# Kernel optimization log

Hardware: AMD Instinct MI355X
Metric: run time of the kernel (lower is better)

## Reference

```python
import jax, jax.numpy as jnp
import numpy as np

N = 4096   # nodes
D = 512    # feature dim
E = 65536  # edges
HOPS = 10  # APPNP K (init arg 'hops')
ALPHA = 0.5


def setup_inputs() -> dict:
    key = jax.random.key(0)
    k1, k2, k3 = jax.random.split(key, 3)
    x_train = jax.random.normal(k1, (N, D), dtype=jnp.float32)
    # kernel_scale = nn.Linear(D, 1, bias=False) weight, flattened to [D]
    w = jax.random.normal(k2, (D,), dtype=jnp.float32) * 0.05
    edge_index = jax.random.randint(k3, (2, E), 0, N, dtype=jnp.int32)
    return {"x_train": x_train, "w": w, "edge_index": edge_index}


def appnp(x0, src, dst, hops, alpha):
    # torch_geometric APPNP with gcn_norm (add self-loops, symmetric norm), dropout=0
    n = x0.shape[0]
    loop = jnp.arange(n, dtype=src.dtype)
    s = jnp.concatenate([src, loop])
    d = jnp.concatenate([dst, loop])
    deg = jax.ops.segment_sum(jnp.ones_like(s, dtype=x0.dtype), d, num_segments=n)
    dis = deg ** -0.5  # deg >= 1 thanks to self-loops
    norm = dis[s] * dis[d]

    def body(h, _):
        agg = jax.ops.segment_sum(norm[:, None] * h[s], d, num_segments=n)
        return (1.0 - alpha) * agg + alpha * x0, None

    h, _ = jax.lax.scan(body, x0, None, length=hops)
    return h


def reference(x_train, w, edge_index):
    n = x_train.shape[0]
    # RBF_kernel: K[i,j] = sum_d w_d * (x_i - x_j)_d^2 for i != j, diag = 1 (the eye)
    xw = x_train * w                                   # [N, D]
    sq = jnp.sum(xw * x_train, axis=1)                 # [N] weighted squared norms
    K = sq[:, None] + sq[None, :] - 2.0 * (xw @ x_train.T)  # [N, N]
    idx = jnp.arange(n)
    K = K.at[idx, idx].set(1.0)

    src, dst = edge_index[0], edge_index[1]
    kgg = appnp(K, src, dst, HOPS, ALPHA)
    kgg = appnp(kgg.T, src, dst, HOPS, ALPHA)

    # adj = dense coo(edge_index, ones); diag = (diag(adj.sum(dim=1)) + 1) ** -0.5
    # (adds 1 to the WHOLE matrix, so off-diagonal entries become 1.0 -- faithful)
    deg_row = jax.ops.segment_sum(jnp.ones((edge_index.shape[1],), K.dtype), src, num_segments=n)
    Dmat = (jnp.diag(deg_row) + 1.0) ** -0.5           # [N, N]
    kgg = Dmat * kgg       # elementwise, as in the original
    kgg = Dmat * kgg.T
    return kgg
```

## Files before the change

### kernel.cpp

```cpp
#include <hip/hip_runtime.h>
#include <stdint.h>

#define Nn 4096
#define Dd 512
#define Ee 65536
#define HOPS 10
#define TPB 512
#define RPT (Nn / TPB)
#define CT8 8
#define WCAP 64
#define KEXT 1536
#define YC 640
#define XK 8192
#define NTMM 88

typedef short bf16x8 __attribute__((ext_vector_type(8)));
typedef float f32x4 __attribute__((ext_vector_type(4)));

__device__ __forceinline__ unsigned short bf16r(float x) {
  unsigned int b = __float_as_uint(x);
  return (unsigned short)((b + 0x7FFFu + ((b >> 16) & 1u)) >> 16);
}
__device__ __forceinline__ unsigned int pkbf(float lo, float hi) {
  return (unsigned int)bf16r(lo) | ((unsigned int)bf16r(hi) << 16);
}
__device__ __forceinline__ float ubf(unsigned short h) {
  return __uint_as_float(((unsigned int)h) << 16);
}
__device__ __forceinline__ void gld16(const unsigned short* g, unsigned short* lds) {
  __builtin_amdgcn_global_load_lds(
      (const __attribute__((address_space(1))) unsigned int*)g,
      (__attribute__((address_space(3))) unsigned int*)lds, 16, 0, 0);
}

__global__ __launch_bounds__(256) void k_sq(const float* __restrict__ x,
                                            const float* __restrict__ w,
                                            float* __restrict__ sq) {
  int row = blockIdx.x;
  int tid = threadIdx.x;
  const float* xr = x + (size_t)row * Dd;
  float partial = 0.f;
  for (int d = tid; d < Dd; d += 256) {
    float xv = xr[d];
    partial += xv * xv * w[d];
  }
  for (int off = 32; off >= 1; off >>= 1) partial += __shfl_down(partial, off, 64);
  __shared__ float red[4];
  int wv = tid >> 6, ln = tid & 63;
  if (ln == 0) red[wv] = partial;
  __syncthreads();
  if (tid == 0) sq[row] = red[0] + red[1] + red[2] + red[3];
}

__global__ void k_count(const int* __restrict__ src, const int* __restrict__ dst,
                        int* __restrict__ degi, int* __restrict__ degrow) {
  int e = blockIdx.x * blockDim.x + threadIdx.x;
  if (e < Ee) {
    atomicAdd(&degi[dst[e]], 1);
    atomicAdd(&degrow[src[e]], 1);
  }
}

__global__ void k_dis(const int* __restrict__ degi, const int* __restrict__ degrow,
                      float* __restrict__ dis, float* __restrict__ d2) {
  int i = blockIdx.x * 256 + threadIdx.x;
  dis[i] = rsqrtf((float)(degi[i] + 1));
  d2[i] = 1.0f / ((float)degrow[i] + 1.0f);
}

__global__ void k_hist(const int* __restrict__ degi, int* __restrict__ binbase) {
  __shared__ int h[WCAP + 1];
  int t = threadIdx.x;
  if (t <= WCAP) h[t] = 0;
  __syncthreads();
  for (int i = t; i < Nn; i += 256) {
    int d = degi[i] + 1;
    if (d > WCAP) d = WCAP;
    atomicAdd(&h[d], 1);
  }
  __syncthreads();
  if (t == 0) {
    int run = 0;
    for (int b = 0; b <= WCAP; b++) { int c = h[b]; binbase[b] = run; run += c; }
  }
}

__global__ void k_scatter(const int* __restrict__ degi, const int* __restrict__ binbase,
                          int* __restrict__ bincnt, int* __restrict__ perm,
                          int* __restrict__ rnk) {
  int i = blockIdx.x * 256 + threadIdx.x;
  int d = degi[i] + 1;
  if (d > WCAP) d = WCAP;
  int pos = binbase[d] + atomicAdd(&bincnt[d], 1);
  perm[pos] = i;
  rnk[i] = pos;
}

__global__ void k_wsub(const int* __restrict__ degi, const int* __restrict__ perm,
                       int* __restrict__ wsub) {
  int t = threadIdx.x;
  int d = degi[perm[t * 64 + 63]] + 1;
  wsub[t] = d > WCAP ? WCAP : d;
}

__global__ void k_fill_ell(const int* __restrict__ src, const int* __restrict__ dst,
                           const float* __restrict__ dis, const int* __restrict__ rnk,
                           int* __restrict__ slot, int2* __restrict__ ell) {
  int i = blockIdx.x * blockDim.x + threadIdx.x;
  if (i < Ee) {
    int s = src[i], d = dst[i];
    int p = atomicAdd(&slot[d], 1);
    if (p < WCAP) ell[(size_t)p * Nn + rnk[d]] = make_int2(s, __float_as_int(dis[s] * dis[d]));
  } else if (i < Ee + Nn) {
    int v = i - Ee;
    int p = atomicAdd(&slot[v], 1);
    if (p < WCAP) ell[(size_t)p * Nn + rnk[v]] = make_int2(v, __float_as_int(dis[v] * dis[v]));
  }
}

__global__ __launch_bounds__(256) void k_xpose(const float* __restrict__ x,
                                               unsigned short* __restrict__ xb) {
  __shared__ float tile[32][33];
  int cx = blockIdx.x, rx = blockIdx.y;
  int t = threadIdx.x, txc = t & 31, tyc = t >> 5;
#pragma unroll
  for (int i = 0; i < 4; i++) {
    int a = tyc + i * 8;
    tile[a][txc] = x[(size_t)(rx * 32 + a) * Dd + cx * 32 + txc];
  }
  __syncthreads();
#pragma unroll
  for (int i = 0; i < 4; i++) {
    int a = tyc + i * 8;
    int c = cx * 32 + a;
    float v = tile[txc][a];
    unsigned short hi = bf16r(v);
    xb[(size_t)c * XK + rx * 32 + txc] = hi;
    xb[(size_t)c * XK + Nn + rx * 32 + txc] = bf16r(v - ubf(hi));
  }
}

__global__ void k_tail(const float* __restrict__ sq, unsigned short* __restrict__ xb) {
  int r = blockIdx.x * 256 + threadIdx.x;
  float v = sq[r];
  unsigned short hi = bf16r(v);
  xb[(size_t)512 * XK + r] = hi;
  xb[(size_t)512 * XK + Nn + r] = bf16r(v - ubf(hi));
  xb[(size_t)513 * XK + r] = bf16r(1.0f);
  xb[(size_t)513 * XK + Nn + r] = 0;
}

__global__ __launch_bounds__(TPB, 4) void k_appnp(unsigned short* __restrict__ mb,
                                                  const int2* __restrict__ ell,
                                                  const int* __restrict__ perm,
                                                  const int* __restrict__ wsub) {
  extern __shared__ uint4 h4u[];
  int j0 = blockIdx.x * CT8;
  int tid = threadIdx.x;
  int wv = tid >> 6, ln = tid & 63;
  int qb = wv * 512 + ln;

#pragma unroll
  for (int rr = 0; rr < RPT; rr++) {
    int r = tid + rr * TPB;
    uint4 v = make_uint4(0u, 0u, 0u, 0u);
    int c = r - j0;
    if (c >= 0 && c < 8) {
      unsigned int one = (c & 1) ? 0x3F800000u : 0x00003F80u;
      if ((c >> 1) == 0) v.x = one;
      else if ((c >> 1) == 1) v.y = one;
      else if ((c >> 1) == 2) v.z = one;
      else v.w = one;
    }
    h4u[r] = v;
  }

  int ws[RPT];
#pragma unroll
  for (int rr = 0; rr < RPT; rr++)
    ws[rr] = __builtin_amdgcn_readfirstlane(wsub[wv * 8 + rr]);
  const int Wv = ws[RPT - 1];

  int rp[RPT], x0c[RPT];
#pragma unroll
  for (int rr = 0; rr < RPT; rr++) {
    rp[rr] = perm[qb + rr * 64];
    int c = rp[rr] - j0;
    x0c[rr] = (c >= 0 && c < 8) ? c : -1;
  }
  __syncthreads();

  for (int it = 0; it < HOPS; it++) {
    int2 cur[RPT];
#pragma unroll
    for (int rr = 0; rr < RPT; rr++) cur[rr] = ell[qb + rr * 64];
    float acc[RPT][8];
#pragma unroll
    for (int rr = 0; rr < RPT; rr++)
#pragma unroll
      for (int c = 0; c < 8; c++) acc[rr][c] = (x0c[rr] == c) ? 1.0f : 0.0f;
    for (int s = 0; s < Wv; s++) {
      int sn = s + 1;
      int2 nxt[RPT];
#pragma unroll
      for (int rr = 0; rr < RPT; rr++)
        if (sn < ws[rr]) nxt[rr] = ell[(size_t)sn * Nn + qb + rr * 64];
#pragma unroll
      for (int rr = 0; rr < RPT; rr++)
        if (s < ws[rr]) {
          float vv = __int_as_float(cur[rr].y);
          uint4 hu = h4u[cur[rr].x];
          acc[rr][0] = fmaf(vv, __uint_as_float(hu.x << 16), acc[rr][0]);
          acc[rr][1] = fmaf(vv, __uint_as_float(hu.x & 0xFFFF0000u), acc[rr][1]);
          acc[rr][2] = fmaf(vv, __uint_as_float(hu.y << 16), acc[rr][2]);
          acc[rr][3] = fmaf(vv, __uint_as_float(hu.y & 0xFFFF0000u), acc[rr][3]);
          acc[rr][4] = fmaf(vv, __uint_as_float(hu.z << 16), acc[rr][4]);
          acc[rr][5] = fmaf(vv, __uint_as_float(hu.z & 0xFFFF0000u), acc[rr][5]);
          acc[rr][6] = fmaf(vv, __uint_as_float(hu.w << 16), acc[rr][6]);
          acc[rr][7] = fmaf(vv, __uint_as_float(hu.w & 0xFFFF0000u), acc[rr][7]);
        }
#pragma unroll
      for (int rr = 0; rr < RPT; rr++)
        if (sn < ws[rr]) cur[rr] = nxt[rr];
    }
    __syncthreads();
#pragma unroll
    for (int rr = 0; rr < RPT; rr++) {
      uint4 v;
      v.x = pkbf(0.5f * acc[rr][0], 0.5f * acc[rr][1]);
      v.y = pkbf(0.5f * acc[rr][2], 0.5f * acc[rr][3]);
      v.z = pkbf(0.5f * acc[rr][4], 0.5f * acc[rr][5]);
      v.w = pkbf(0.5f * acc[rr][6], 0.5f * acc[rr][7]);
      h4u[rp[rr]] = v;
    }
    __syncthreads();
  }

#pragma unroll
  for (int rr = 0; rr < RPT; rr++) {
    int r = tid + rr * TPB;
    *(uint4*)&mb[(size_t)r * Nn + j0] = h4u[r];
  }
}

__device__ __forceinline__ void mm_step(const unsigned short* __restrict__ Ap, int lda,
                                        const unsigned short* __restrict__ Bp, int ldb,
                                        unsigned short* As, unsigned short* Bs,
                                        int i0, int j0, int k0, int l, int w, int wr,
                                        int wc, f32x4 acc[4][4]) {
  int rsub = w * 8 + (l >> 3);
  int scg = ((l & 7) ^ (l >> 3)) * 8;
#pragma unroll
  for (int r = 0; r < 4; r++) {
    int row = r * 32 + rsub;
    gld16(Ap + (size_t)(i0 + row) * lda + k0 + scg, As + (r * 32 + w * 8) * 64);
    gld16(Bp + (size_t)(j0 + row) * ldb + k0 + scg, Bs + (r * 32 + w * 8) * 64);
  }
  __syncthreads();
#pragma unroll
  for (int q = 0; q < 2; q++) {
    bf16x8 af[4], bg[4];
#pragma unroll
    for (int m = 0; m < 4; m++) {
      int ar = wr * 64 + m * 16 + (l & 15);
      af[m] = *(const bf16x8*)(As + ar * 64 + ((((l >> 4) + 4 * q) ^ (ar & 7)) * 8));
      int br = wc * 64 + m * 16 + (l & 15);
      bg[m] = *(const bf16x8*)(Bs + br * 64 + ((((l >> 4) + 4 * q) ^ (br & 7)) * 8));
    }
#pragma unroll
    for (int m = 0; m < 4; m++)
#pragma unroll
      for (int n = 0; n < 4; n++)
        acc[m][n] = __builtin_amdgcn_mfma_f32_16x16x32_bf16(af[m], bg[n], acc[m][n], 0, 0, 0);
  }
  __syncthreads();
}

__global__ __launch_bounds__(256) void k_ymm(const unsigned short* __restrict__ Mb,
                                             const unsigned short* __restrict__ xb,
                                             const float* __restrict__ wp,
                                             unsigned short* __restrict__ aext,
                                             unsigned short* __restrict__ bext,
                                             float* __restrict__ mu,
                                             float* __restrict__ m1) {
  __shared__ unsigned short As[128 * 64];
  __shared__ unsigned short Bs[128 * 64];
  int i0 = blockIdx.y * 128, j0 = blockIdx.x * 128;
  int tid = threadIdx.x, l = tid & 63, w = tid >> 6;
  int wr = w >> 1, wc = w & 1;
  f32x4 acc[4][4];
#pragma unroll
  for (int m = 0; m < 4; m++)
#pragma unroll
    for (int n = 0; n < 4; n++) acc[m][n] = (f32x4){0.f, 0.f, 0.f, 0.f};

  for (int k0 = 0; k0 < Nn; k0 += 64)
    mm_step(Mb, Nn, xb, XK, As, Bs, i0, j0, k0, l, w, wr, wc, acc);
  for (int k0 = 0; k0 < Nn; k0 += 64)
    mm_step(Mb, Nn, xb + Nn, XK, As, Bs, i0, j0, k0, l, w, wr, wc, acc);

#pragma unroll
  for (int m = 0; m < 4; m++) {
#pragma unroll
    for (int n = 0; n < 4; n++) {
#pragma unroll
      for (int q = 0; q < 4; q++) {
        int gi = i0 + wr * 64 + m * 16 + ((l >> 4) << 2) + q;
        int gj = j0 + wc * 64 + n * 16 + (l & 15);
        float y = acc[m][n][q];
        if (gj < 512) {
          unsigned short yhi = bf16r(y);
          unsigned short ylo = bf16r(y - ubf(yhi));
          float p = -2.f * wp[gj] * y;
          unsigned short phi = bf16r(p);
          unsigned short plo = bf16r(p - ubf(phi));
          bext[(size_t)gi * KEXT + gj] = yhi;
          bext[(size_t)gi * KEXT + 512 + gj] = ylo;
          bext[(size_t)gi * KEXT + 1024 + gj] = yhi;
          aext[(size_t)gi * KEXT + gj] = phi;
          aext[(size_t)gi * KEXT + 512 + gj] = phi;
          aext[(size_t)gi * KEXT + 1024 + gj] = plo;
        } else if (gj == 512) {
          mu[gi] = y;
        } else if (gj == 513) {
          m1[gi] = y;
        }
      }
    }
  }
}

__global__ __launch_bounds__(512, 2) void k_mm2(const unsigned short* __restrict__ Mb,
                                                const unsigned short* __restrict__ Aext,
                                                const unsigned short* __restrict__ Bext,
                                                const float* __restrict__ mu,
                                                const float* __restrict__ m1,
                                                const float* __restrict__ d2,
                                                float* __restrict__ out) {
  extern __shared__ unsigned short sh[];
  int lid = blockIdx.x;
  int swz = (lid & 7) * 32 + (lid >> 3);
  int i0 = (swz >> 4) * 256, j0 = (swz & 15) * 256;
  int tid = threadIdx.x, l = tid & 63, w = tid >> 6;
  int wr = w >> 2, wc = w & 3;
  int rsub = l >> 3;
  int scg = ((l & 7) ^ (l >> 3)) * 8;
  int aRowBase = wr * 128 + wc * 32;
  int bRowBase = (wc >> 1) * 128 + (wr * 2 + (wc & 1)) * 32;

  f32x4 acc[8][4];
#pragma unroll
  for (int m = 0; m < 8; m++)
#pragma unroll
    for (int n = 0; n < 4; n++) acc[m][n] = (f32x4){0.f, 0.f, 0.f, 0.f};

  auto STG = [&](int g, int t, int b) {
    const unsigned short *pa, *pb;
    int lda, kk;
    if (t < 64) { pa = Mb; pb = Mb; lda = Nn; kk = t * 64; }
    else { pa = Aext; pb = Bext; lda = KEXT; kk = (t - 64) * 64; }
    if (g < 4) {
      int r = bRowBase + g * 8;
      gld16(pb + (size_t)(j0 + r + rsub) * lda + kk + scg, sh + 32768 + b * 16384 + r * 64);
    } else {
      int r = aRowBase + (g - 4) * 8;
      gld16(pa + (size_t)(i0 + r + rsub) * lda + kk + scg, sh + b * 16384 + r * 64);
    }
  };

#pragma unroll
  for (int g = 0; g < 8; g++) STG(g, 0, 0);
  asm volatile("s_waitcnt vmcnt(0)" ::: "memory");
  __builtin_amdgcn_s_barrier();

  for (int kt = 0; kt < NTMM; kt++) {
    int cur = kt & 1, nxtb = cur ^ 1;
    const unsigned short* Ac = sh + cur * 16384;
    const unsigned short* Bc = sh + 32768 + cur * 16384;
    bool pre = (kt + 1 < NTMM);
#pragma unroll
    for (int p = 0; p < 4; p++) {
      const int mh = p >> 1, nh = p & 1;
      bf16x8 af[4][2], bg[2][2];
#pragma unroll
      for (int m4 = 0; m4 < 4; m4++) {
        int ar = wr * 128 + (mh * 4 + m4) * 16 + (l & 15);
#pragma unroll
        for (int ks = 0; ks < 2; ks++) {
          int c = ks * 4 + (l >> 4);
          af[m4][ks] = *(const bf16x8*)(Ac + ar * 64 + ((c ^ (ar & 7)) * 8));
        }
      }
#pragma unroll
      for (int n2 = 0; n2 < 2; n2++) {
        int br = wc * 64 + (nh * 2 + n2) * 16 + (l & 15);
#pragma unroll
        for (int ks = 0; ks < 2; ks++) {
          int c = ks * 4 + (l >> 4);
          bg[n2][ks] = *(const bf16x8*)(Bc + br * 64 + ((c ^ (br & 7)) * 8));
        }
      }
      if (pre) {
        if (p == 0) { STG(0, kt + 1, nxtb); STG(1, kt + 1, nxtb); STG(2, kt + 1, nxtb); }
        else if (p == 1) { STG(3, kt + 1, nxtb); STG(4, kt + 1, nxtb); STG(5, kt + 1, nxtb); }
        else if (p == 2) { STG(6, kt + 1, nxtb); STG(7, kt + 1, nxtb); }
      }
      if (p == 3) asm volatile("s_waitcnt vmcnt(0)" ::: "memory");
      __builtin_amdgcn_s_barrier();
      __builtin_amdgcn_s_setprio(1);
#pragma unroll
      for (int m4 = 0; m4 < 4; m4++)
#pragma unroll
        for (int n2 = 0; n2 < 2; n2++)
#pragma unroll
          for (int ks = 0; ks < 2; ks++)
            acc[mh * 4 + m4][nh * 2 + n2] = __builtin_amdgcn_mfma_f32_16x16x32_bf16(
                af[m4][ks], bg[n2][ks], acc[mh * 4 + m4][nh * 2 + n2], 0, 0, 0);
      __builtin_amdgcn_s_setprio(0);
      __builtin_amdgcn_s_barrier();
    }
  }

#pragma unroll
  for (int m = 0; m < 8; m++) {
#pragma unroll
    for (int n = 0; n < 4; n++) {
#pragma unroll
      for (int q = 0; q < 4; q++) {
        int gi = i0 + wr * 128 + m * 16 + ((l >> 4) << 2) + q;
        int gj = j0 + wc * 64 + n * 16 + (l & 15);
        float v = acc[m][n][q] + mu[gi] * m1[gj] + m1[gi] * mu[gj];
        if (gi == gj) v *= d2[gi];
        out[(size_t)gi * Nn + gj] = v;
      }
    }
  }
}

extern "C" void kernel_launch(void* const* d_in, const int* in_sizes, int n_in,
                              void* d_out, int out_size, void* d_ws, size_t ws_size,
                              hipStream_t stream) {
  const float* x = (const float*)d_in[0];
  const float* w = (const float*)d_in[1];
  const int* ei = (const int*)d_in[2];
  const int* src = ei;
  const int* dstv = ei + Ee;
  float* out = (float*)d_out;

  unsigned short* Mb = (unsigned short*)d_ws;
  unsigned short* aext = Mb + (size_t)Nn * Nn;
  unsigned short* bext = aext + (size_t)Nn * KEXT;
  unsigned short* xb = bext + (size_t)Nn * KEXT;
  int2* ell = (int2*)(xb + (size_t)YC * XK);
  float* sq = (float*)(ell + (size_t)WCAP * Nn);
  float* dis = sq + Nn;
  float* d2 = dis + Nn;
  float* mu = d2 + Nn;
  float* m1 = mu + Nn;
  int* degi = (int*)(m1 + Nn);
  int* degrow = degi + Nn;
  int* slotcnt = degrow + Nn;
  int* bincnt = slotcnt + Nn;
  int* binbase = bincnt + (WCAP + 1);
  int* perm = binbase + (WCAP + 1);
  int* rnk = perm + Nn;
  int* wsub = rnk + Nn;

  hipMemsetAsync(ell, 0, (size_t)WCAP * Nn * sizeof(int2), stream);
  hipMemsetAsync(degi, 0, sizeof(int) * (3 * Nn + (WCAP + 1)), stream);
  hipMemsetAsync(xb, 0, (size_t)YC * XK * sizeof(unsigned short), stream);

  k_sq<<<Nn, 256, 0, stream>>>(x, w, sq);
  k_count<<<Ee / 256, 256, 0, stream>>>(src, dstv, degi, degrow);
  k_dis<<<Nn / 256, 256, 0, stream>>>(degi, degrow, dis, d2);
  k_hist<<<1, 256, 0, stream>>>(degi, binbase);
  k_scatter<<<Nn / 256, 256, 0, stream>>>(degi, binbase, bincnt, perm, rnk);
  k_wsub<<<1, 64, 0, stream>>>(degi, perm, wsub);
  k_fill_ell<<<(Ee + Nn + 255) / 256, 256, 0, stream>>>(src, dstv, dis, rnk, slotcnt, ell);
  k_xpose<<<dim3(16, 128), 256, 0, stream>>>(x, xb);
  k_tail<<<Nn / 256, 256, 0, stream>>>(sq, xb);

  k_appnp<<<Nn / CT8, TPB, Nn * sizeof(uint4), stream>>>(Mb, ell, perm, wsub);
  k_ymm<<<dim3(YC / 128, Nn / 128), 256, 0, stream>>>(Mb, xb, w, aext, bext, mu, m1);
  k_mm2<<<256, 512, 131072, stream>>>(Mb, aext, bext, mu, m1, d2, out);
}
```

Before: 865.8 us.

## Store propagated matrix in column-chunked layout and issue all prefetches at once

The APPNP propagation kernel now writes its bf16 output as contiguous 8-column chunks per block, so each block's store is one fully contiguous region instead of rows strided by N. Both matmul kernels' loaders for that matrix are rewritten to address the new chunked layout. The main GEMM also issues all eight next-tile global-to-LDS loads in the first sub-phase instead of spreading them over three. This is meant to coalesce the propagation writes and simplify load scheduling, at the cost of loads that stride across chunks and more loads in flight early in each k-step.

```diff
diff --git a/kernel.cpp b/kernel.cpp
--- a/kernel.cpp
+++ b/kernel.cpp
@@ -32,6 +32,7 @@
       (const __attribute__((address_space(1))) unsigned int*)g,
       (__attribute__((address_space(3))) unsigned int*)lds, 16, 0, 0);
 }
+
 
 __global__ __launch_bounds__(256) void k_sq(const float* __restrict__ x,
                                             const float* __restrict__ w,
@@ -239,11 +240,11 @@
 #pragma unroll
   for (int rr = 0; rr < RPT; rr++) {
     int r = tid + rr * TPB;
-    *(uint4*)&mb[(size_t)r * Nn + j0] = h4u[r];
-  }
-}
-
-__device__ __forceinline__ void mm_step(const unsigned short* __restrict__ Ap, int lda,
+    *(uint4*)&mb[(size_t)blockIdx.x * Nn * 8 + (size_t)r * 8] = h4u[r];
+  }
+}
+
+__device__ __forceinline__ void mm_step(const unsigned short* __restrict__ Mb,
                                         const unsigned short* __restrict__ Bp, int ldb,
                                         unsigned short* As, unsigned short* Bs,
                                         int i0, int j0, int k0, int l, int w, int wr,
@@ -253,7 +254,7 @@
 #pragma unroll
   for (int r = 0; r < 4; r++) {
     int row = r * 32 + rsub;
-    gld16(Ap + (size_t)(i0 + row) * lda + k0 + scg, As + (r * 32 + w * 8) * 64);
+    gld16(Mb + (size_t)(k0 + scg) * Nn + (size_t)(i0 + row) * 8, As + (r * 32 + w * 8) * 64);
     gld16(Bp + (size_t)(j0 + row) * ldb + k0 + scg, Bs + (r * 32 + w * 8) * 64);
   }
   __syncthreads();
@@ -295,9 +296,9 @@
     for (int n = 0; n < 4; n++) acc[m][n] = (f32x4){0.f, 0.f, 0.f, 0.f};
 
   for (int k0 = 0; k0 < Nn; k0 += 64)
-    mm_step(Mb, Nn, xb, XK, As, Bs, i0, j0, k0, l, w, wr, wc, acc);
+    mm_step(Mb, xb, XK, As, Bs, i0, j0, k0, l, w, wr, wc, acc);
   for (int k0 = 0; k0 < Nn; k0 += 64)
-    mm_step(Mb, Nn, xb + Nn, XK, As, Bs, i0, j0, k0, l, w, wr, wc, acc);
+    mm_step(Mb, xb + Nn, XK, As, Bs, i0, j0, k0, l, w, wr, wc, acc);
 
 #pragma unroll
   for (int m = 0; m < 4; m++) {
@@ -355,16 +356,26 @@
     for (int n = 0; n < 4; n++) acc[m][n] = (f32x4){0.f, 0.f, 0.f, 0.f};
 
   auto STG = [&](int g, int t, int b) {
-    const unsigned short *pa, *pb;
-    int lda, kk;
-    if (t < 64) { pa = Mb; pb = Mb; lda = Nn; kk = t * 64; }
-    else { pa = Aext; pb = Bext; lda = KEXT; kk = (t - 64) * 64; }
-    if (g < 4) {
-      int r = bRowBase + g * 8;
-      gld16(pb + (size_t)(j0 + r + rsub) * lda + kk + scg, sh + 32768 + b * 16384 + r * 64);
+    if (t < 64) {
+      int kk = t * 64;
+      if (g < 4) {
+        int r = bRowBase + g * 8;
+        gld16(Mb + (size_t)(kk + scg) * Nn + (size_t)(j0 + r + rsub) * 8,
+              sh + 32768 + b * 16384 + r * 64);
+      } else {
+        int r = aRowBase + (g - 4) * 8;
+        gld16(Mb + (size_t)(kk + scg) * Nn + (size_t)(i0 + r + rsub) * 8,
+              sh + b * 16384 + r * 64);
+      }
     } else {
-      int r = aRowBase + (g - 4) * 8;
-      gld16(pa + (size_t)(i0 + r + rsub) * lda + kk + scg, sh + b * 16384 + r * 64);
+      int kk = (t - 64) * 64;
+      if (g < 4) {
+        int r = bRowBase + g * 8;
+        gld16(Bext + (size_t)(j0 + r + rsub) * KEXT + kk + scg, sh + 32768 + b * 16384 + r * 64);
+      } else {
+        int r = aRowBase + (g - 4) * 8;
+        gld16(Aext + (size_t)(i0 + r + rsub) * KEXT + kk + scg, sh + b * 16384 + r * 64);
+      }
     }
   };
 
@@ -400,10 +411,9 @@
           bg[n2][ks] = *(const bf16x8*)(Bc + br * 64 + ((c ^ (br & 7)) * 8));
         }
       }
-      if (pre) {
-        if (p == 0) { STG(0, kt + 1, nxtb); STG(1, kt + 1, nxtb); STG(2, kt + 1, nxtb); }
-        else if (p == 1) { STG(3, kt + 1, nxtb); STG(4, kt + 1, nxtb); STG(5, kt + 1, nxtb); }
-        else if (p == 2) { STG(6, kt + 1, nxtb); STG(7, kt + 1, nxtb); }
+      if (pre && p == 0) {
+#pragma unroll
+        for (int g = 0; g < 8; g++) STG(g, kt + 1, nxtb);
       }
       if (p == 3) asm volatile("s_waitcnt vmcnt(0)" ::: "memory");
       __builtin_amdgcn_s_barrier();
```

New measurement: 921.3 us. 6.4% more time.
